# Performance work log

Hardware: AMD Instinct MI355X
Metric: run time of the kernel (lower is better)

The kernel has to match this reference:

```python
import jax, jax.numpy as jnp
import numpy as np

N = 100000
E = 1250000
D = 64
R = 16


def _glorot(key, shape):
    fan_in, fan_out = shape[-2], shape[-1]
    lim = jnp.sqrt(6.0 / (fan_in + fan_out))
    return jax.random.uniform(key, shape, jnp.float32, -lim, lim)


def setup_inputs() -> dict:
    key = jax.random.key(0)
    ks = jax.random.split(key, 9)
    x = jax.random.normal(ks[0], (N, D), jnp.float32)
    edge_index = jax.random.randint(ks[1], (2, E), 0, N, jnp.int64 if jax.config.jax_enable_x64 else jnp.int32).astype(jnp.int32)
    edge_type = jax.random.randint(ks[2], (E,), 0, R).astype(jnp.int32)
    return {
        "x": x,
        "edge_index": edge_index,
        "edge_type": edge_type,
        "W1": _glorot(ks[3], (R, D, D)),
        "sw1": _glorot(ks[4], (D, D)),
        "b1": jnp.zeros((D,), jnp.float32),
        "W2": _glorot(ks[5], (R, D, D)),
        "sw2": _glorot(ks[6], (D, D)),
        "b2": jnp.zeros((D,), jnp.float32),
    }


def _rgcn_layer(x, src, dst, edge_type, W, sw, b, residual):
    # self transform [N, O]
    out = x @ sw
    # per-relation transform of all nodes: [N, R, O] (avoids [E, D, O] gathered weights,
    # same math as bmm(x_j, W[edge_type]))
    xW = jnp.einsum('nd,rdo->nro', x, W)
    msg = xW[src, edge_type]                      # [E, O] per-edge messages
    agg = jax.ops.segment_sum(msg, dst, num_segments=N)  # scatter-add aggregate
    out = out + agg
    if residual:
        out = out + x  # Identity residual (in == out channels)
    out = out + b
    return jax.nn.relu(out)


def reference(x, edge_index, edge_type, W1, sw1, b1, W2, sw2, b2):
    src, dst = edge_index[0], edge_index[1]
    # layer 1: residual=True; layer 2: encoding=False -> no residual.
    # activation (relu) applied after every layer by RGCN.forward; dropout p=0 / eval -> no-op.
    h = _rgcn_layer(x, src, dst, edge_type, W1, sw1, b1, residual=True)
    h = _rgcn_layer(h, src, dst, edge_type, W2, sw2, b2, residual=False)
    return h
```

## Files before the change

kernel.cpp:

```cpp
#include <hip/hip_runtime.h>
#include <hip/hip_bf16.h>

#define NN 100000
#define NE 1250000
#define DD 64
#define RR 16
#define NTILE 6250
#define NBINS 100000
#define NBLK_SCAN 391
#define CAPROWS 224
#define DLCAP 576

typedef __attribute__((ext_vector_type(8))) short s16x8;
typedef __attribute__((ext_vector_type(4))) float f32x4;

static __device__ __forceinline__ unsigned short f2bf(float v) {
    __hip_bfloat16 h = __float2bfloat16(v);
    return __builtin_bit_cast(unsigned short, h);
}
static __device__ __forceinline__ unsigned int pack2(float a, float b) {
    return ((unsigned int)f2bf(b) << 16) | (unsigned int)f2bf(a);
}


__global__ void hist_key(const int* __restrict__ dst, const int* __restrict__ et,
                         int* __restrict__ cnt) {
    int e = blockIdx.x * 256 + threadIdx.x;
    if (e < NE) atomicAdd(&cnt[(dst[e] >> 4) * 16 + et[e]], 1);
}

__global__ __launch_bounds__(256) void scan1(const int* __restrict__ cnt,
                                             int* __restrict__ rp, int* __restrict__ part) {
    __shared__ int s[256];
    int i = blockIdx.x * 256 + threadIdx.x;
    int v = (i < NBINS) ? cnt[i] : 0;
    s[threadIdx.x] = v;
    __syncthreads();
    for (int off = 1; off < 256; off <<= 1) {
        int t = (threadIdx.x >= off) ? s[threadIdx.x - off] : 0;
        __syncthreads();
        s[threadIdx.x] += t;
        __syncthreads();
    }
    if (i < NBINS) rp[i] = s[threadIdx.x] - v;
    if (threadIdx.x == 255) part[blockIdx.x] = s[255];
}

__global__ void scan2(int* __restrict__ part, int* __restrict__ rp) {
    __shared__ int s[NBLK_SCAN];
    if (threadIdx.x < NBLK_SCAN) s[threadIdx.x] = part[threadIdx.x];
    __syncthreads();
    if (threadIdx.x == 0) {
        int acc = 0;
        for (int b = 0; b < NBLK_SCAN; ++b) { int t = s[b]; s[b] = acc; acc += t; }
        rp[NBINS] = NE;
    }
    __syncthreads();
    if (threadIdx.x < NBLK_SCAN) part[threadIdx.x] = s[threadIdx.x];
}

__global__ void scan3(int* __restrict__ rp, const int* __restrict__ part, int* __restrict__ cur) {
    int i = blockIdx.x * 256 + threadIdx.x;
    if (i < NBINS) {
        int v = rp[i] + part[blockIdx.x];
        rp[i] = v;
        cur[i] = v;
    }
}

__global__ void scatter_key(const int* __restrict__ src, const int* __restrict__ dst,
                            const int* __restrict__ et, int* __restrict__ cur,
                            unsigned int* __restrict__ ep) {
    int e = blockIdx.x * 256 + threadIdx.x;
    if (e >= NE) return;
    int d = dst[e];
    int p = atomicAdd(&cur[(d >> 4) * 16 + et[e]], 1);
    ep[p] = (unsigned int)src[e] | ((unsigned int)(d & 15) << 20);
}


__global__ void prep_w2(const float* __restrict__ W1, const float* __restrict__ sw1,
                        const float* __restrict__ W2, const float* __restrict__ sw2,
                        unsigned short* __restrict__ wt) {
    int i = blockIdx.x * 256 + threadIdx.x;
    if (i >= 2 * 17 * DD * DD) return;
    int d = i & 63;
    int o = (i >> 6) & 63;
    int p = (i >> 12) % 17;
    int l = i / (17 * DD * DD);
    const float* srcp;
    if (p < 16) srcp = (l ? W2 : W1) + p * DD * DD;
    else        srcp = (l ? sw2 : sw1);
    wt[i] = f2bf(srcp[d * DD + o]);
}

__global__ void prep_x2(const float* __restrict__ x, unsigned short* __restrict__ xb) {
    int i = blockIdx.x * blockDim.x + threadIdx.x;
    if (i < NN * DD) xb[i] = f2bf(x[i]);
}

__global__ __launch_bounds__(256, 4) void fused_layer(
    const unsigned short* __restrict__ xb,
    const unsigned short* __restrict__ wt,
    const int* __restrict__ rp,
    const unsigned int* __restrict__ ep,
    const float* __restrict__ bias,
    const float* __restrict__ xres,
    unsigned short* __restrict__ outb,
    float* __restrict__ outf)
{
    __shared__ __attribute__((aligned(16))) unsigned char Ash[CAPROWS * 128];
    __shared__ __attribute__((aligned(8)))  unsigned char dlb[DLCAP + 32];

    const int tid  = threadIdx.x;
    const int wid  = tid >> 6;
    const int lane = tid & 63;
    const int c = lane & 15;
    const int q = lane >> 4;
    const int tile = blockIdx.x;
    const int n0 = tile * 16;

    int rpv = 0;
    if (lane < 17) rpv = rp[tile * 16 + lane];
    const int e0  = __shfl(rpv, 0, 64);
    const int cnt = __shfl(rpv, 16, 64) - e0;

    {
        const int lim = cnt < DLCAP ? cnt : DLCAP;
        for (int i = tid; i < lim; i += 256)
            dlb[i] = (unsigned char)(ep[e0 + i] >> 20);
        if (tid < 32) {
            int p = lim + tid;
            if (p < DLCAP + 32) dlb[p] = 0xFF;
        }
    }
    {
        const int nrows = cnt < CAPROWS ? cnt : CAPROWS;
        const int half = tid & 1;
        for (int i = tid >> 1; i < nrows; i += 128) {
            int src = (int)(ep[e0 + i] & 0xFFFFF);
            const unsigned short* xr = xb + (size_t)src * DD + half * 32;
            s16x8 v0 = *(const s16x8*)(xr);
            s16x8 v1 = *(const s16x8*)(xr + 8);
            s16x8 v2 = *(const s16x8*)(xr + 16);
            s16x8 v3 = *(const s16x8*)(xr + 24);
            unsigned char* bp = Ash + i * 128;
            const int h8 = (i & 7);
            *(s16x8*)(bp + (((half * 4 + 0) ^ h8) * 16)) = v0;
            *(s16x8*)(bp + (((half * 4 + 1) ^ h8) * 16)) = v1;
            *(s16x8*)(bp + (((half * 4 + 2) ^ h8) * 16)) = v2;
            *(s16x8*)(bp + (((half * 4 + 3) ^ h8) * 16)) = v3;
        }
    }
    __syncthreads();

    const bool dlOK = (cnt <= DLCAP);
    const int och = wid * 16 + c;
    const unsigned short* wbase = wt + (size_t)och * DD + q * 8;
    const short one = (short)0x3F80;

    auto plane_body = [&](int r, s16x8 W0, s16x8 W1, f32x4& Dst) {
        const int s0 = __shfl(rpv, r, 64);
        const int s1 = __shfl(rpv, r + 1, 64);
        for (int b0 = s0; b0 < s1; b0 += 16) {
            const int rem = s1 - b0;
            const int lbase = b0 - e0;

            unsigned da;
            if (dlOK) {
                const unsigned* dl32 = (const unsigned*)dlb;
                int idx = lbase + q * 4;
                int w = idx >> 2;
                int sh = (idx & 3) * 8;
                unsigned long long pa =
                    ((unsigned long long)dl32[w + 1] << 32) | dl32[w];
                da = (unsigned)(pa >> sh);
            } else {
                int eA = min(b0 + c, s1 - 1);
                unsigned wa = ep[eA];
                int dl = (b0 + c < s1) ? (int)(wa >> 20) : 31;
                unsigned x0 = (unsigned)__shfl(dl, q * 4 + 0, 64) & 255u;
                unsigned x1 = (unsigned)__shfl(dl, q * 4 + 1, 64) & 255u;
                unsigned x2 = (unsigned)__shfl(dl, q * 4 + 2, 64) & 255u;
                unsigned x3 = (unsigned)__shfl(dl, q * 4 + 3, 64) & 255u;
                da = x0 | (x1 << 8) | (x2 << 16) | (x3 << 24);
            }
            s16x8 a2;
            #pragma unroll
            for (int j = 0; j < 4; ++j) {
                int jj = q * 4 + j;
                a2[j] = ((int)((da >> (8 * j)) & 255) == c && jj < rem) ? one : (short)0;
                a2[j + 4] = 0;
            }

            int rA = min(b0 + c, s1 - 1) - e0;
            s16x8 a0, a1;
            if (rA < CAPROWS) {
                const unsigned char* ap = Ash + rA * 128;
                const int off = (q ^ (rA & 7)) * 16;
                a0 = *(const s16x8*)(ap + off);
                a1 = *(const s16x8*)(ap + (off ^ 64));
            } else {
                int src = (int)(ep[e0 + rA] & 0xFFFFF);
                const unsigned short* xr = xb + (size_t)src * DD + q * 8;
                a0 = *(const s16x8*)(xr);
                a1 = *(const s16x8*)(xr + 32);
            }

            __builtin_amdgcn_s_setprio(1);
            f32x4 cA = {0.f, 0.f, 0.f, 0.f};
            cA = __builtin_amdgcn_mfma_f32_16x16x32_bf16(a0, W0, cA, 0, 0, 0);
            cA = __builtin_amdgcn_mfma_f32_16x16x32_bf16(a1, W1, cA, 0, 0, 0);
            s16x8 bv;
            #pragma unroll
            for (int j = 0; j < 4; ++j) {
                bv[j]     = (short)f2bf(cA[j]);
                bv[j + 4] = 0;
            }
            Dst = __builtin_amdgcn_mfma_f32_16x16x32_bf16(a2, bv, Dst, 0, 0, 0);
            __builtin_amdgcn_s_setprio(0);
        }
    };

    s16x8 wc0 = *(const s16x8*)(wbase);
    s16x8 wc1 = *(const s16x8*)(wbase + 32);
    f32x4 D0 = {0.f, 0.f, 0.f, 0.f};
    f32x4 D1 = {0.f, 0.f, 0.f, 0.f};

    for (int rr = 0; rr < 8; ++rr) {
        const int r = rr * 2;
        const unsigned short* p1 = wbase + (size_t)(r + 1) * (DD * DD);
        s16x8 wn0 = *(const s16x8*)(p1);
        s16x8 wn1 = *(const s16x8*)(p1 + 32);
        plane_body(r, wc0, wc1, D0);
        const int r2 = (r + 2 <= 16) ? r + 2 : 16;
        const unsigned short* p2 = wbase + (size_t)r2 * (DD * DD);
        s16x8 t0 = *(const s16x8*)(p2);
        s16x8 t1 = *(const s16x8*)(p2 + 32);
        plane_body(r + 1, wn0, wn1, D1);
        wc0 = t0; wc1 = t1;
    }

    {
        const unsigned short* xr = xb + (size_t)(n0 + c) * DD + q * 8;
        s16x8 a0 = *(const s16x8*)(xr);
        s16x8 a1 = *(const s16x8*)(xr + 32);
        D0 = __builtin_amdgcn_mfma_f32_16x16x32_bf16(a0, wc0, D0, 0, 0, 0);
        D1 = __builtin_amdgcn_mfma_f32_16x16x32_bf16(a1, wc1, D1, 0, 0, 0);
    }
    f32x4 Dacc = D0 + D1;

    const float bc = bias[och];
    #pragma unroll
    for (int v = 0; v < 4; ++v) {
        const int node = n0 + q * 4 + v;
        float val = Dacc[v] + bc;
        if (xres) val += xres[(size_t)node * DD + och];
        val = fmaxf(val, 0.f);
        if (outf) outf[(size_t)node * DD + och] = val;
        if (outb) {
            float nb = __shfl_xor(val, 1, 64);
            if (!(c & 1))
                *(unsigned int*)(outb + (size_t)node * DD + och) = pack2(val, nb);
        }
    }
}


extern "C" void kernel_launch(void* const* d_in, const int* in_sizes, int n_in,
                              void* d_out, int out_size, void* d_ws, size_t ws_size,
                              hipStream_t stream)
{
    (void)in_sizes; (void)n_in; (void)out_size; (void)ws_size;
    const float* x    = (const float*)d_in[0];
    const int*   ei   = (const int*)d_in[1];
    const int*   et   = (const int*)d_in[2];
    const float* W1   = (const float*)d_in[3];
    const float* sw1  = (const float*)d_in[4];
    const float* b1   = (const float*)d_in[5];
    const float* W2   = (const float*)d_in[6];
    const float* sw2  = (const float*)d_in[7];
    const float* b2   = (const float*)d_in[8];
    float* out = (float*)d_out;

    const int* srcA = ei;
    const int* dstA = ei + NE;

    char* ws = (char*)d_ws;
    unsigned short* xb   = (unsigned short*)(ws);
    unsigned short* h1b  = (unsigned short*)(ws + 12800000);
    unsigned short* wt2  = (unsigned short*)(ws + 25600000);
    unsigned int*   ep   = (unsigned int*)(ws + 25878528);
    int*            rp   = (int*)(ws + 30878528);
    int*            cnt  = (int*)(ws + 31278544);
    int*            cur  = (int*)(ws + 31678544);
    int*            part = (int*)(ws + 32078544);

    const int NB_E    = (NE + 255) / 256;
    const int NB_ELEM = (NN * DD + 255) / 256;
    const int WPL = 17 * DD * DD;

    hipMemsetAsync(cnt, 0, NBINS * sizeof(int), stream);
    hist_key<<<NB_E, 256, 0, stream>>>(dstA, et, cnt);
    scan1<<<NBLK_SCAN, 256, 0, stream>>>(cnt, rp, part);
    scan2<<<1, 512, 0, stream>>>(part, rp);
    scan3<<<NBLK_SCAN, 256, 0, stream>>>(rp, part, cur);
    scatter_key<<<NB_E, 256, 0, stream>>>(srcA, dstA, et, cur, ep);

    prep_w2<<<(2 * 17 * DD * DD + 255) / 256, 256, 0, stream>>>(W1, sw1, W2, sw2, wt2);
    prep_x2<<<NB_ELEM, 256, 0, stream>>>(x, xb);

    fused_layer<<<NTILE, 256, 0, stream>>>(xb, wt2, rp, ep, b1, x, h1b, nullptr);
    fused_layer<<<NTILE, 256, 0, stream>>>(h1b, wt2 + WPL, rp, ep, b2, nullptr, nullptr, out);
}
```

Baseline: 527.2 us.

## Precompute per-relation node transforms densely, then gather-aggregate per destination node

Adds a dense path used when the workspace is large enough. A GEMM kernel computes x@W_r for all 16 relations, plus the self weight, for every node into a bf16 buffer of 17 planes. Edges are re-sorted by destination only, and a per-node kernel gathers and sums the precomputed rows. This replaces the fused per-tile kernel, which recomputed transforms per edge and used masked MFMAs for the scatter. The trade is a large extra write and random gather traffic, plus rounding the messages to bf16 before accumulation. The change also removes the setprio hints from the fallback fused kernel.

```diff
diff --git a/kernel.cpp b/kernel.cpp
--- a/kernel.cpp
+++ b/kernel.cpp
@@ -2,6 +2,7 @@
 #include <hip/hip_bf16.h>
 
 #define NN 100000
+#define NNP 100032
 #define NE 1250000
 #define DD 64
 #define RR 16
@@ -21,12 +22,40 @@
 static __device__ __forceinline__ unsigned int pack2(float a, float b) {
     return ((unsigned int)f2bf(b) << 16) | (unsigned int)f2bf(a);
 }
-
+static __device__ __forceinline__ float bf2f(unsigned short u) {
+    unsigned int x = ((unsigned int)u) << 16;
+    return __builtin_bit_cast(float, x);
+}
+
+
+__global__ void hist_dst(const int* __restrict__ dst, int* __restrict__ cnt) {
+    int e = blockIdx.x * 256 + threadIdx.x;
+    if (e < NE) atomicAdd(&cnt[dst[e]], 1);
+}
+
+__global__ void scatter_dst(const int* __restrict__ src, const int* __restrict__ dst,
+                            const int* __restrict__ et, int* __restrict__ cur,
+                            unsigned int* __restrict__ ep) {
+    int e = blockIdx.x * 256 + threadIdx.x;
+    if (e >= NE) return;
+    int p = atomicAdd(&cur[dst[e]], 1);
+    ep[p] = (unsigned int)src[e] | ((unsigned int)et[e] << 20);
+}
 
 __global__ void hist_key(const int* __restrict__ dst, const int* __restrict__ et,
                          int* __restrict__ cnt) {
     int e = blockIdx.x * 256 + threadIdx.x;
     if (e < NE) atomicAdd(&cnt[(dst[e] >> 4) * 16 + et[e]], 1);
+}
+
+__global__ void scatter_key(const int* __restrict__ src, const int* __restrict__ dst,
+                            const int* __restrict__ et, int* __restrict__ cur,
+                            unsigned int* __restrict__ ep) {
+    int e = blockIdx.x * 256 + threadIdx.x;
+    if (e >= NE) return;
+    int d = dst[e];
+    int p = atomicAdd(&cur[(d >> 4) * 16 + et[e]], 1);
+    ep[p] = (unsigned int)src[e] | ((unsigned int)(d & 15) << 20);
 }
 
 __global__ __launch_bounds__(256) void scan1(const int* __restrict__ cnt,
@@ -66,16 +95,6 @@
         rp[i] = v;
         cur[i] = v;
     }
-}
-
-__global__ void scatter_key(const int* __restrict__ src, const int* __restrict__ dst,
-                            const int* __restrict__ et, int* __restrict__ cur,
-                            unsigned int* __restrict__ ep) {
-    int e = blockIdx.x * 256 + threadIdx.x;
-    if (e >= NE) return;
-    int d = dst[e];
-    int p = atomicAdd(&cur[(d >> 4) * 16 + et[e]], 1);
-    ep[p] = (unsigned int)src[e] | ((unsigned int)(d & 15) << 20);
 }
 
 
@@ -97,6 +116,84 @@
 __global__ void prep_x2(const float* __restrict__ x, unsigned short* __restrict__ xb) {
     int i = blockIdx.x * blockDim.x + threadIdx.x;
     if (i < NN * DD) xb[i] = f2bf(x[i]);
+}
+
+__global__ __launch_bounds__(256) void xw_gemm(const unsigned short* __restrict__ xin,
+                                               const unsigned short* __restrict__ wt,
+                                               unsigned short* __restrict__ xwb) {
+    const int tid  = threadIdx.x;
+    const int wid  = tid >> 6;
+    const int lane = tid & 63;
+    const int c = lane & 15;
+    const int q = lane >> 4;
+    const int n0 = blockIdx.x * 64 + wid * 16;
+
+    const unsigned short* xr = xin + (size_t)(n0 + c) * DD + q * 8;
+    s16x8 b0 = *(const s16x8*)(xr);
+    s16x8 b1 = *(const s16x8*)(xr + 32);
+
+    #pragma unroll 2
+    for (int p = 0; p < 17; ++p) {
+        const unsigned short* wp = wt + (size_t)p * (DD * DD) + q * 8;
+        unsigned short* orow = xwb + ((size_t)p * NNP + n0 + c) * DD + q * 4;
+        #pragma unroll
+        for (int ob = 0; ob < 4; ++ob) {
+            const unsigned short* wrow = wp + (size_t)(ob * 16 + c) * DD;
+            s16x8 a0 = *(const s16x8*)(wrow);
+            s16x8 a1 = *(const s16x8*)(wrow + 32);
+            f32x4 acc = {0.f, 0.f, 0.f, 0.f};
+            acc = __builtin_amdgcn_mfma_f32_16x16x32_bf16(a0, b0, acc, 0, 0, 0);
+            acc = __builtin_amdgcn_mfma_f32_16x16x32_bf16(a1, b1, acc, 0, 0, 0);
+            uint2 val;
+            val.x = pack2(acc[0], acc[1]);
+            val.y = pack2(acc[2], acc[3]);
+            *(uint2*)(orow + ob * 16) = val;
+        }
+    }
+}
+
+__global__ __launch_bounds__(256) void aggregate(
+    const unsigned short* __restrict__ xwb,
+    const int* __restrict__ rp,
+    const unsigned int* __restrict__ ep,
+    const float* __restrict__ bias,
+    const float* __restrict__ xres,
+    unsigned short* __restrict__ outb,
+    float* __restrict__ outf)
+{
+    const int tid  = threadIdx.x;
+    const int wid  = tid >> 6;
+    const int lane = tid & 63;
+    const int n = blockIdx.x * 4 + wid;
+    if (n >= NN) return;
+
+    const int s0 = rp[n];
+    const int s1 = rp[n + 1];
+
+    float acc = bf2f(xwb[((size_t)16 * NNP + n) * DD + lane]);
+    acc += bias[lane];
+    if (xres) acc += xres[(size_t)n * DD + lane];
+
+    for (int base = s0; base < s1; base += 16) {
+        unsigned wv[16];
+        #pragma unroll
+        for (int k = 0; k < 16; ++k)
+            wv[k] = ep[min(base + k, s1 - 1)];
+        const int m = s1 - base;
+        #pragma unroll
+        for (int k = 0; k < 16; ++k) {
+            if (k < m) {
+                const unsigned w = wv[k];
+                const unsigned short* rb =
+                    xwb + ((size_t)(w >> 20) * NNP + (w & 0xFFFFFu)) * DD;
+                acc += bf2f(rb[lane]);
+            }
+        }
+    }
+
+    acc = fmaxf(acc, 0.f);
+    if (outb) outb[(size_t)n * DD + lane] = f2bf(acc);
+    if (outf) outf[(size_t)n * DD + lane] = acc;
 }
 
 __global__ __launch_bounds__(256, 4) void fused_layer(
@@ -165,7 +262,6 @@
         for (int b0 = s0; b0 < s1; b0 += 16) {
             const int rem = s1 - b0;
             const int lbase = b0 - e0;
-
             unsigned da;
             if (dlOK) {
                 const unsigned* dl32 = (const unsigned*)dlb;
@@ -192,7 +288,6 @@
                 a2[j] = ((int)((da >> (8 * j)) & 255) == c && jj < rem) ? one : (short)0;
                 a2[j + 4] = 0;
             }
-
             int rA = min(b0 + c, s1 - 1) - e0;
             s16x8 a0, a1;
             if (rA < CAPROWS) {
@@ -206,8 +301,6 @@
                 a0 = *(const s16x8*)(xr);
                 a1 = *(const s16x8*)(xr + 32);
             }
-
-            __builtin_amdgcn_s_setprio(1);
             f32x4 cA = {0.f, 0.f, 0.f, 0.f};
             cA = __builtin_amdgcn_mfma_f32_16x16x32_bf16(a0, W0, cA, 0, 0, 0);
             cA = __builtin_amdgcn_mfma_f32_16x16x32_bf16(a1, W1, cA, 0, 0, 0);
@@ -218,7 +311,6 @@
                 bv[j + 4] = 0;
             }
             Dst = __builtin_amdgcn_mfma_f32_16x16x32_bf16(a2, bv, Dst, 0, 0, 0);
-            __builtin_amdgcn_s_setprio(0);
         }
     };
 
@@ -240,7 +332,6 @@
         plane_body(r + 1, wn0, wn1, D1);
         wc0 = t0; wc1 = t1;
     }
-
     {
         const unsigned short* xr = xb + (size_t)(n0 + c) * DD + q * 8;
         s16x8 a0 = *(const s16x8*)(xr);
@@ -271,7 +362,7 @@
                               void* d_out, int out_size, void* d_ws, size_t ws_size,
                               hipStream_t stream)
 {
-    (void)in_sizes; (void)n_in; (void)out_size; (void)ws_size;
+    (void)in_sizes; (void)n_in; (void)out_size;
     const float* x    = (const float*)d_in[0];
     const int*   ei   = (const int*)d_in[1];
     const int*   et   = (const int*)d_in[2];
@@ -295,21 +386,43 @@
     int*            cnt  = (int*)(ws + 31278544);
     int*            cur  = (int*)(ws + 31678544);
     int*            part = (int*)(ws + 32078544);
+    const size_t XWB_OFF = 32080640;
+    unsigned short* xwb  = (unsigned short*)(ws + XWB_OFF);
+    const size_t REQ = XWB_OFF + (size_t)17 * NNP * DD * 2;
 
     const int NB_E    = (NE + 255) / 256;
     const int NB_ELEM = (NN * DD + 255) / 256;
     const int WPL = 17 * DD * DD;
 
+    const bool dense = (ws_size >= REQ);
+
     hipMemsetAsync(cnt, 0, NBINS * sizeof(int), stream);
-    hist_key<<<NB_E, 256, 0, stream>>>(dstA, et, cnt);
-    scan1<<<NBLK_SCAN, 256, 0, stream>>>(cnt, rp, part);
-    scan2<<<1, 512, 0, stream>>>(part, rp);
-    scan3<<<NBLK_SCAN, 256, 0, stream>>>(rp, part, cur);
-    scatter_key<<<NB_E, 256, 0, stream>>>(srcA, dstA, et, cur, ep);
+    if (dense) {
+        hist_dst<<<NB_E, 256, 0, stream>>>(dstA, cnt);
+        scan1<<<NBLK_SCAN, 256, 0, stream>>>(cnt, rp, part);
+        scan2<<<1, 512, 0, stream>>>(part, rp);
+        scan3<<<NBLK_SCAN, 256, 0, stream>>>(rp, part, cur);
+        scatter_dst<<<NB_E, 256, 0, stream>>>(srcA, dstA, et, cur, ep);
+    } else {
+        hist_key<<<NB_E, 256, 0, stream>>>(dstA, et, cnt);
+        scan1<<<NBLK_SCAN, 256, 0, stream>>>(cnt, rp, part);
+        scan2<<<1, 512, 0, stream>>>(part, rp);
+        scan3<<<NBLK_SCAN, 256, 0, stream>>>(rp, part, cur);
+        scatter_key<<<NB_E, 256, 0, stream>>>(srcA, dstA, et, cur, ep);
+    }
 
     prep_w2<<<(2 * 17 * DD * DD + 255) / 256, 256, 0, stream>>>(W1, sw1, W2, sw2, wt2);
     prep_x2<<<NB_ELEM, 256, 0, stream>>>(x, xb);
 
-    fused_layer<<<NTILE, 256, 0, stream>>>(xb, wt2, rp, ep, b1, x, h1b, nullptr);
-    fused_layer<<<NTILE, 256, 0, stream>>>(h1b, wt2 + WPL, rp, ep, b2, nullptr, nullptr, out);
-}
+    if (dense) {
+        const int NB_G = (NN + 63) / 64;
+        const int NB_A = (NN + 3) / 4;
+        xw_gemm<<<NB_G, 256, 0, stream>>>(xb, wt2, xwb);
+        aggregate<<<NB_A, 256, 0, stream>>>(xwb, rp, ep, b1, x, h1b, nullptr);
+        xw_gemm<<<NB_G, 256, 0, stream>>>(h1b, wt2 + WPL, xwb);
+        aggregate<<<NB_A, 256, 0, stream>>>(xwb, rp, ep, b2, nullptr, nullptr, out);
+    } else {
+        fused_layer<<<NTILE, 256, 0, stream>>>(xb, wt2, rp, ep, b1, x, h1b, nullptr);
+        fused_layer<<<NTILE, 256, 0, stream>>>(h1b, wt2 + WPL, rp, ep, b2, nullptr, nullptr, out);
+    }
+}
```

Result: slower. 673.9 us (+27.8%).
